# Optimization experiments

Measured on AMD Instinct MI355X. Metric: run time of the kernel, lower is better.

Reference implementation:

```python
import jax, jax.numpy as jnp
import numpy as np

B, N, CS, CZ, CH, H, PQ, PV = 1, 768, 384, 128, 16, 12, 4, 8
INF, EPS, LN_EPS = 1e5, 1e-8, 1e-5


def setup_inputs() -> dict:
    key = jax.random.key(0)
    ks = jax.random.split(key, 16)
    def nrm(k, shape, scale=0.02):
        return jax.random.normal(k, shape, dtype=jnp.float32) * scale
    return {
        "s": jax.random.normal(ks[0], (B, N, CS), jnp.float32),
        "z": jax.random.normal(ks[1], (B, N, N, CZ), jnp.float32),
        "r_rot": jax.random.normal(ks[2], (B, N, 5, 3, 3), jnp.float32),
        "r_trans": jax.random.normal(ks[3], (B, N, 5, 3), jnp.float32),
        "mask": jnp.ones((B, N, 5), jnp.float32),
        "wq": nrm(ks[4], (H * CH, CS)), "bq": jnp.zeros((H * CH,), jnp.float32),
        "wkv": nrm(ks[5], (2 * H * CH, CS)), "bkv": jnp.zeros((2 * H * CH,), jnp.float32),
        "wqp": nrm(ks[6], (H * PQ * 3, CS)), "bqp": jnp.zeros((H * PQ * 3,), jnp.float32),
        "wkvp": nrm(ks[7], (H * (PQ + PV) * 3, CS)), "bkvp": jnp.zeros((H * (PQ + PV) * 3,), jnp.float32),
        "wb": nrm(ks[8], (H, CZ)), "bb": jnp.zeros((H,), jnp.float32),
        "head_w": nrm(ks[9], (H,), 0.5),
        "wout": nrm(ks[10], (CS, H * (CZ + CH + PV * 4))), "bout": jnp.zeros((CS,), jnp.float32),
        "wexp": nrm(ks[11], (5 * CS, CS)), "bexp": jnp.zeros((5 * CS,), jnp.float32),
        "ln_g": jnp.ones((CS,), jnp.float32), "ln_b": jnp.zeros((CS,), jnp.float32),
        "ww": nrm(ks[12], (1, CS)), "bw": jnp.zeros((1,), jnp.float32),
    }


def _mix(x, fg_mask, weight, ndims):
    # x: [B,N,5,...]; weighted blend of backbone frame (index 0) and mean of
    # masked functional-group frames (indices 1:5).
    bb_f = x[:, :, :1]
    m = fg_mask.reshape(fg_mask.shape + (1,) * ndims)
    fg = (x[:, :, 1:] * m).sum(axis=2, keepdims=True)
    denom = fg_mask.sum(-1, keepdims=True).reshape(fg_mask.shape[:2] + (1,) * (ndims + 1))
    fg = fg / (denom + 1e-8)
    w = weight.reshape(weight.shape[:2] + (1,) * (ndims + 1))
    return (w * bb_f + (1.0 - w) * fg)[:, :, 0]


def _ipa(s, z, r_rot, r_trans, mask, wq, bq, wkv, bkv, wqp, bqp, wkvp, bkvp,
         wb, bb, head_w, wout, bout, wexp, bexp, ln_g, ln_b, ww, bw):
    fg_mask = mask[..., 1:]            # [B,N,4]
    ulr = mask[..., 0]                 # [B,N]
    # softmax over a size-1 axis (as in original code -> all ones)
    weight = jax.nn.softmax(s @ ww.T + bw, axis=-1)   # [B,N,1]

    se = (s @ wexp.T + bexp).reshape(B, N, 5, CS)
    mu = se.mean(-1, keepdims=True)
    var = ((se - mu) ** 2).mean(-1, keepdims=True)
    se = (se - mu) * jax.lax.rsqrt(var + LN_EPS) * ln_g + ln_b

    q = _mix((se @ wq.T + bq).reshape(B, N, 5, H, CH), fg_mask, weight, 2)      # [B,N,H,CH]
    kv = _mix((se @ wkv.T + bkv).reshape(B, N, 5, H, 2 * CH), fg_mask, weight, 2)
    k, v = kv[..., :CH], kv[..., CH:]

    def pts_of(w_, b_, npts):
        lin = se @ w_.T + b_                                   # [B,N,5,3*H*npts]
        pts = jnp.moveaxis(lin.reshape(B, N, 5, 3, H * npts), -2, -1)  # [B,N,5,H*npts,3]
        pts = jnp.einsum('bnfij,bnfpj->bnfpi', r_rot, pts) + r_trans[:, :, :, None, :]
        return _mix(pts.reshape(B, N, 5, H, npts, 3), fg_mask, weight, 3)

    q_pts = pts_of(wqp, bqp, PQ)                               # [B,N,H,PQ,3]
    kv_pts = pts_of(wkvp, bkvp, PQ + PV)
    k_pts, v_pts = kv_pts[..., :PQ, :], kv_pts[..., PQ:, :]

    bias = z @ wb.T + bb                                       # [B,N,N,H]
    a = jnp.einsum('bihc,bjhc->bhij', q, k) * (1.0 / (3 * CH)) ** 0.5
    a = a + (1.0 / 3.0) ** 0.5 * jnp.transpose(bias, (0, 3, 1, 2))

    d2 = jnp.sum((q_pts[:, :, None] - k_pts[:, None]) ** 2, axis=-1)  # [B,N,N,H,PQ]
    hw = jax.nn.softplus(head_w) * (1.0 / (3 * (PQ * 9.0 / 2))) ** 0.5
    pt_att = -0.5 * jnp.sum(d2 * hw[:, None], axis=-1)         # [B,N,N,H]
    a = a + jnp.transpose(pt_att, (0, 3, 1, 2))
    sq_mask = INF * (ulr[:, :, None] * ulr[:, None, :] - 1.0)
    a = jax.nn.softmax(a + sq_mask[:, None], axis=-1)          # [B,H,N,N]

    o = jnp.einsum('bhij,bjhc->bihc', a, v).reshape(B, N, H * CH)
    o_pt = jnp.einsum('bhij,bjhpx->bihpx', a, v_pts)           # [B,N,H,PV,3]
    rot0, t0 = r_rot[:, :, 0], r_trans[:, :, 0]                # backbone frame
    # invert_apply: R^T (x - t)
    o_pt = jnp.einsum('bnik,bnhpi->bnhpk', rot0, o_pt - t0[:, :, None, None, :])
    o_pt_norm = jnp.sqrt(jnp.sum(o_pt ** 2, -1) + EPS).reshape(B, N, H * PV)
    o_pt = o_pt.reshape(B, N, H * PV, 3)
    o_pair = jnp.einsum('bhij,bijc->bihc', a, z).reshape(B, N, H * CZ)
    cat = jnp.concatenate([o, o_pt[..., 0], o_pt[..., 1], o_pt[..., 2], o_pt_norm, o_pair], -1)
    return cat @ wout.T + bout                                 # [B,N,CS]


def reference(s, z, r_rot, r_trans, mask, wq, bq, wkv, bkv, wqp, bqp, wkvp, bkvp,
              wb, bb, head_w, wout, bout, wexp, bexp, ln_g, ln_b, ww, bw):
    return _ipa(s, z, r_rot, r_trans, mask, wq, bq, wkv, bkv, wqp, bqp, wkvp, bkvp,
                wb, bb, head_w, wout, bout, wexp, bexp, ln_g, ln_b, ww, bw)
```

## Files before the change

kernel.cpp:

```cpp
#include <hip/hip_runtime.h>
#include <stdint.h>


typedef float f32x4 __attribute__((ext_vector_type(4)));
typedef short s16x8 __attribute__((ext_vector_type(8)));

__device__ __forceinline__ float bf2f(unsigned short u) {
    union { unsigned int i; float f; } v; v.i = ((unsigned int)u) << 16; return v.f;
}
__device__ __forceinline__ float bf2fs(short s) { return bf2f((unsigned short)s); }
__device__ __forceinline__ unsigned short f2bf(float f) {
    union { float f; unsigned int i; } v; v.f = f;
    unsigned int r = v.i + 0x7fffu + ((v.i >> 16) & 1u);
    return (unsigned short)(r >> 16);
}

__global__ __launch_bounds__(256) void k_se(
    const float* __restrict__ s, const float* __restrict__ wexp,
    const float* __restrict__ bexp, const float* __restrict__ ln_g,
    const float* __restrict__ ln_b, float* __restrict__ se0)
{
    const int n0 = blockIdx.x * 4;
    const int t  = threadIdx.x;
    __shared__ float se_l[4 * 384];
    __shared__ float mu_s[4], rs_s[4];

    const bool has1 = (t < 128);
    const float* wr0 = wexp + (size_t)t * 384;
    const float* wr1 = wexp + (size_t)(t + 256) * 384;
    float a0[4] = {0.f,0.f,0.f,0.f}, a1[4] = {0.f,0.f,0.f,0.f};

    for (int k4 = 0; k4 < 96; ++k4) {
        f32x4 sv[4];
        #pragma unroll
        for (int r = 0; r < 4; ++r)
            sv[r] = *(const f32x4*)(s + (size_t)(n0 + r) * 384 + k4 * 4);
        f32x4 w0 = *(const f32x4*)(wr0 + k4 * 4);
        #pragma unroll
        for (int m = 0; m < 4; ++m) {
            float wv = w0[m];
            #pragma unroll
            for (int r = 0; r < 4; ++r) a0[r] += sv[r][m] * wv;
        }
        if (has1) {
            f32x4 w1 = *(const f32x4*)(wr1 + k4 * 4);
            #pragma unroll
            for (int m = 0; m < 4; ++m) {
                float wv = w1[m];
                #pragma unroll
                for (int r = 0; r < 4; ++r) a1[r] += sv[r][m] * wv;
            }
        }
    }
    {
        float b0 = bexp[t];
        #pragma unroll
        for (int r = 0; r < 4; ++r) se_l[r * 384 + t] = a0[r] + b0;
        if (has1) {
            float b1 = bexp[t + 256];
            #pragma unroll
            for (int r = 0; r < 4; ++r) se_l[r * 384 + t + 256] = a1[r] + b1;
        }
    }
    __syncthreads();
    {
        const int w = t >> 6, lane = t & 63;
        float s1 = 0.f, s2 = 0.f;
        #pragma unroll
        for (int q = 0; q < 6; ++q) {
            float v = se_l[w * 384 + lane + q * 64];
            s1 += v; s2 += v * v;
        }
        for (int mk = 1; mk < 64; mk <<= 1) {
            s1 += __shfl_xor(s1, mk, 64);
            s2 += __shfl_xor(s2, mk, 64);
        }
        if (lane == 0) {
            float mu = s1 * (1.f / 384.f);
            float var = s2 * (1.f / 384.f) - mu * mu;
            mu_s[w] = mu;
            rs_s[w] = rsqrtf(fmaxf(var, 0.f) + 1e-5f);
        }
    }
    __syncthreads();
    for (int x = t; x < 4 * 384; x += 256) {
        int r = x / 384, c = x - r * 384;
        se0[(size_t)(n0 + r) * 384 + c] = (se_l[x] - mu_s[r]) * rs_s[r] * ln_g[c] + ln_b[c];
    }
}

__device__ __forceinline__ void wmap(int c,
    const float* wq, const float* bq, const float* wkv, const float* bkv,
    const float* wqp, const float* bqp, const float* wkvp, const float* bkvp,
    const float** w, float* b)
{
    if (c < 192)      { *w = wq   + (size_t)c * 384;         *b = bq[c]; }
    else if (c < 576) { *w = wkv  + (size_t)(c - 192) * 384; *b = bkv[c - 192]; }
    else if (c < 720) { *w = wqp  + (size_t)(c - 576) * 384; *b = bqp[c - 576]; }
    else              { *w = wkvp + (size_t)(c - 720) * 384; *b = bkvp[c - 720]; }
}

__global__ __launch_bounds__(256) void k_proj(
    const float* __restrict__ se0,
    const float* __restrict__ wq,  const float* __restrict__ bq,
    const float* __restrict__ wkv, const float* __restrict__ bkv,
    const float* __restrict__ wqp, const float* __restrict__ bqp,
    const float* __restrict__ wkvp,const float* __restrict__ bkvp,
    const float* __restrict__ r_rot, const float* __restrict__ r_trans,
    float* __restrict__ q_out, unsigned short* __restrict__ k_out,
    unsigned short* __restrict__ v_out, float* __restrict__ qp_out,
    unsigned short* __restrict__ kp_out, unsigned short* __restrict__ vp_out,
    float* __restrict__ k2_out)
{
    const int n0 = blockIdx.x * 8;
    const int cb = blockIdx.y;
    const int t  = threadIdx.x;
    const int cbase = cb * 576;
    __shared__ float lin[8 * 576];
    __shared__ float kprot[8 * 144];

    const bool has2 = (t < 64);
    const float *w0p, *w1p, *w2p; float b0, b1, b2;
    wmap(cbase + t,        wq, bq, wkv, bkv, wqp, bqp, wkvp, bkvp, &w0p, &b0);
    wmap(cbase + t + 256,  wq, bq, wkv, bkv, wqp, bqp, wkvp, bkvp, &w1p, &b1);
    if (has2) wmap(cbase + t + 512, wq, bq, wkv, bkv, wqp, bqp, wkvp, bkvp, &w2p, &b2);
    else { w2p = wq; b2 = 0.f; }

    float ac0[8] = {}, ac1[8] = {}, ac2[8] = {};
    for (int k4 = 0; k4 < 96; ++k4) {
        f32x4 sv[8];
        #pragma unroll
        for (int r = 0; r < 8; ++r)
            sv[r] = *(const f32x4*)(se0 + (size_t)(n0 + r) * 384 + k4 * 4);
        f32x4 wv0 = *(const f32x4*)(w0p + k4 * 4);
        f32x4 wv1 = *(const f32x4*)(w1p + k4 * 4);
        #pragma unroll
        for (int m = 0; m < 4; ++m) {
            float a = wv0[m], b = wv1[m];
            #pragma unroll
            for (int r = 0; r < 8; ++r) { ac0[r] += sv[r][m] * a; ac1[r] += sv[r][m] * b; }
        }
        if (has2) {
            f32x4 wv2 = *(const f32x4*)(w2p + k4 * 4);
            #pragma unroll
            for (int m = 0; m < 4; ++m) {
                float a = wv2[m];
                #pragma unroll
                for (int r = 0; r < 8; ++r) ac2[r] += sv[r][m] * a;
            }
        }
    }
    #pragma unroll
    for (int r = 0; r < 8; ++r) {
        lin[r * 576 + t]       = ac0[r] + b0;
        lin[r * 576 + t + 256] = ac1[r] + b1;
    }
    if (has2) {
        #pragma unroll
        for (int r = 0; r < 8; ++r) lin[r * 576 + t + 512] = ac2[r] + b2;
    }
    __syncthreads();

    if (cb == 0) {
        for (int x = t; x < 8 * 576; x += 256) {
            int r = x / 576, lc = x - r * 576;
            int n = n0 + r;
            float v = lin[x];
            if (lc < 192) q_out[(size_t)n * 192 + lc] = v;
            else {
                int l2 = lc - 192, h = l2 >> 5, c = l2 & 31;
                if (c < 16) k_out[(size_t)n * 192 + h * 16 + c] = f2bf(v);
                else        v_out[(size_t)n * 192 + h * 16 + (c - 16)] = f2bf(v);
            }
        }
    } else {
        for (int x = t; x < 8 * 576; x += 256) {
            int r = x / 576, y = x - r * 576;
            int pt = y / 3, i = y - pt * 3;
            int n = n0 + r;
            const float* rot = r_rot + (size_t)n * 45;
            float t0 = r_trans[(size_t)n * 15 + i];
            float v;
            if (pt < 48) {
                v = rot[i*3+0] * lin[r*576 + pt]
                  + rot[i*3+1] * lin[r*576 + 48 + pt]
                  + rot[i*3+2] * lin[r*576 + 96 + pt] + t0;
                qp_out[(size_t)n * 144 + pt * 3 + i] = v;
            } else {
                int pp = pt - 48;
                v = rot[i*3+0] * lin[r*576 + 144 + pp]
                  + rot[i*3+1] * lin[r*576 + 288 + pp]
                  + rot[i*3+2] * lin[r*576 + 432 + pp] + t0;
                int h = pp / 12, pl = pp - h * 12;
                if (pl < 4) {
                    kp_out[(size_t)n * 144 + (h * 4 + pl) * 3 + i] = f2bf(v);
                    kprot[r * 144 + (h * 4 + pl) * 3 + i] = v;
                } else {
                    vp_out[(size_t)n * 288 + (h * 8 + (pl - 4)) * 3 + i] = f2bf(v);
                }
            }
        }
        __syncthreads();
        if (t < 96) {
            int r = t / 12, h = t - r * 12;
            float ss = 0.f;
            #pragma unroll
            for (int d = 0; d < 12; ++d) {
                float v = kprot[r * 144 + h * 12 + d];
                ss += v * v;
            }
            k2_out[(size_t)(n0 + r) * 12 + h] = ss;
        }
    }
}

__global__ __launch_bounds__(256) void k_attn(
    const float* __restrict__ z, const float* __restrict__ mask,
    const float* __restrict__ head_w, const float* __restrict__ wb,
    const float* __restrict__ bb,
    const float* __restrict__ r_rot, const float* __restrict__ r_trans,
    const float* __restrict__ q_ws, const float* __restrict__ qp_ws,
    const float* __restrict__ k2_ws,
    const unsigned short* __restrict__ k_bf, const unsigned short* __restrict__ v_bf,
    const unsigned short* __restrict__ kp_bf, const unsigned short* __restrict__ vp_bf,
    float* __restrict__ cat)
{
    const int i = blockIdx.x;
    const int t = threadIdx.x;
    const int lane = t & 63, wv = t >> 6;
    const int quad = lane >> 4, lcol = lane & 15;

    __shared__ short zb[64 * 136];
    __shared__ short kt[64 * 200];
    __shared__ short kpt[64 * 146];
    __shared__ float L[64 * 17];
    __shared__ float Pt[16 * 68];
    __shared__ float qs[192], qps[144];
    __shared__ float K2t[64 * 13], ulrt[64];
    __shared__ float m_s[16], l_s[16], alph_s[16], linv_s[16];
    __shared__ float cpt[16], cbbb[16], q2s[16];
    __shared__ float optb[288];

    const float c_qk = 0.14433756729740643f;
    const float c_b  = 0.57735026918962576f;

    if (t < 192) qs[t]  = q_ws[(size_t)i * 192 + t];
    if (t < 144) qps[t] = qp_ws[(size_t)i * 144 + t];
    if (t < 16) { m_s[t] = -1e30f; l_s[t] = 0.f; alph_s[t] = 1.f; }
    if (t < 16) {
        if (t < 12) {
            float x = head_w[t];
            float sp = logf(1.f + __expf(x));
            cpt[t]  = -0.5f * sp * 0.13608276348795434f;
            cbbb[t] = c_b * bb[t];
        } else { cpt[t] = 0.f; cbbb[t] = 0.f; }
    }
    for (int x = t; x < 4 * 68; x += 256) Pt[12 * 68 + x] = 0.f;
    const float ulr_i = mask[(size_t)i * 5];

    s16x8 wbf[4];
    #pragma unroll
    for (int kb = 0; kb < 4; ++kb) {
        #pragma unroll
        for (int j = 0; j < 8; ++j) {
            int c = kb * 32 + quad * 8 + j;
            wbf[kb][j] = (lcol < 12) ? (short)f2bf(wb[(size_t)lcol * 128 + c]) : (short)0;
        }
    }
    __syncthreads();
    if (t < 16) {
        if (t < 12) {
            float ss = 0.f;
            #pragma unroll
            for (int d = 0; d < 12; ++d) { float v = qps[t * 12 + d]; ss += v * v; }
            q2s[t] = ss;
        } else q2s[t] = 0.f;
    }

    f32x4 acc_op[2] = { {0.f,0.f,0.f,0.f}, {0.f,0.f,0.f,0.f} };
    f32x4 acc_s = {0.f,0.f,0.f,0.f};
    int role_h = -1;
    if (t < 48) role_h = t >> 2;
    else if (t >= 64 && t < 136) role_h = ((t - 64) * 4) / 24;

    for (int jt = 0; jt < 12; ++jt) {
        const int j0 = jt * 64;
        __syncthreads();

        {
            const float* zrow = z + (size_t)i * 98304 + (size_t)j0 * 128;
            #pragma unroll
            for (int s = 0; s < 8; ++s) {
                int idx = t + s * 256;
                f32x4 v = *(const f32x4*)(zrow + idx * 4);
                int jl = idx >> 5, c4 = (idx & 31) * 4;
                uint2 pk;
                pk.x = (unsigned)f2bf(v[0]) | ((unsigned)f2bf(v[1]) << 16);
                pk.y = (unsigned)f2bf(v[2]) | ((unsigned)f2bf(v[3]) << 16);
                *(uint2*)&zb[jl * 136 + c4] = pk;
            }
            const uint4* ksrc = (const uint4*)(k_bf + (size_t)j0 * 192);
            #pragma unroll
            for (int s = 0; s < 6; ++s) {
                int idx = t + s * 256;
                uint4 vk = ksrc[idx];
                int jl = idx / 24, c = (idx - jl * 24) * 8;
                *(uint4*)&kt[jl * 200 + c] = vk;
            }
            const uint2* kpsrc = (const uint2*)(kp_bf + (size_t)j0 * 144);
            #pragma unroll
            for (int s = 0; s < 9; ++s) {
                int idx = t + s * 256;
                uint2 vk = kpsrc[idx];
                int jl = idx / 36, c = (idx - jl * 36) * 4;
                *(unsigned int*)&kpt[jl * 146 + c]     = vk.x;
                *(unsigned int*)&kpt[jl * 146 + c + 2] = vk.y;
            }
            #pragma unroll
            for (int s = 0; s < 3; ++s) {
                int x = t + s * 256;
                int jl = x / 12, h = x - jl * 12;
                K2t[jl * 13 + h] = k2_ws[(size_t)j0 * 12 + x];
            }
            if (t < 64) ulrt[t] = mask[(size_t)(j0 + t) * 5];
        }
        __syncthreads();

        {
            f32x4 d = {0.f,0.f,0.f,0.f};
            #pragma unroll
            for (int kb = 0; kb < 4; ++kb) {
                s16x8 a = *(const s16x8*)&zb[(wv * 16 + lcol) * 136 + kb * 32 + quad * 8];
                d = __builtin_amdgcn_mfma_f32_16x16x32_bf16(a, wbf[kb], d, 0, 0, 0);
            }
            if (lcol < 12) {
                #pragma unroll
                for (int r = 0; r < 4; ++r)
                    L[(wv * 16 + quad * 4 + r) * 17 + lcol] = c_b * d[r] + cbbb[lcol];
            }
        }
        __syncthreads();

        #pragma unroll
        for (int es = 0; es < 3; ++es) {
            int e = t + es * 256;
            int h = e >> 6, jl = e & 63;
            f32x4 qv0 = *(const f32x4*)&qs[h * 16];
            f32x4 qv1 = *(const f32x4*)&qs[h * 16 + 4];
            f32x4 qv2 = *(const f32x4*)&qs[h * 16 + 8];
            f32x4 qv3 = *(const f32x4*)&qs[h * 16 + 12];
            s16x8 k0 = *(const s16x8*)&kt[jl * 200 + h * 16];
            s16x8 k1 = *(const s16x8*)&kt[jl * 200 + h * 16 + 8];
            float qk = 0.f;
            #pragma unroll
            for (int m = 0; m < 4; ++m) {
                qk += qv0[m] * bf2fs(k0[m]);
                qk += qv1[m] * bf2fs(k0[4 + m]);
                qk += qv2[m] * bf2fs(k1[m]);
                qk += qv3[m] * bf2fs(k1[4 + m]);
            }
            float dp = 0.f;
            #pragma unroll
            for (int dd = 0; dd < 6; ++dd) {
                unsigned int u = *(const unsigned int*)&kpt[jl * 146 + h * 12 + dd * 2];
                dp += qps[h * 12 + dd * 2]     * bf2f((unsigned short)(u & 0xffffu));
                dp += qps[h * 12 + dd * 2 + 1] * bf2f((unsigned short)(u >> 16));
            }
            float ptt = cpt[h] * (q2s[h] + K2t[jl * 13 + h] - 2.f * dp);
            float lg = c_qk * qk + ptt + 1e5f * (ulr_i * ulrt[jl] - 1.f);
            L[jl * 17 + h] += lg;
        }
        __syncthreads();

        if (t < 192) {
            int h = t >> 4, u = t & 15;
            float v0 = L[(u * 4 + 0) * 17 + h];
            float v1 = L[(u * 4 + 1) * 17 + h];
            float v2 = L[(u * 4 + 2) * 17 + h];
            float v3 = L[(u * 4 + 3) * 17 + h];
            float mx = fmaxf(fmaxf(v0, v1), fmaxf(v2, v3));
            for (int mk = 1; mk < 16; mk <<= 1) mx = fmaxf(mx, __shfl_xor(mx, mk, 16));
            float mold = m_s[h];
            float mnew = fmaxf(mold, mx);
            float w0 = __expf(v0 - mnew), w1 = __expf(v1 - mnew);
            float w2 = __expf(v2 - mnew), w3 = __expf(v3 - mnew);
            Pt[h * 68 + u * 4 + 0] = w0;
            Pt[h * 68 + u * 4 + 1] = w1;
            Pt[h * 68 + u * 4 + 2] = w2;
            Pt[h * 68 + u * 4 + 3] = w3;
            float sm = w0 + w1 + w2 + w3;
            for (int mk = 1; mk < 16; mk <<= 1) sm += __shfl_xor(sm, mk, 16);
            if (u == 0) {
                float al = __expf(mold - mnew);
                m_s[h] = mnew; alph_s[h] = al;
                l_s[h] = l_s[h] * al + sm;
            }
        }
        __syncthreads();

        {
            float al[4];
            #pragma unroll
            for (int r = 0; r < 4; ++r) al[r] = alph_s[quad * 4 + r];
            #pragma unroll
            for (int nt = 0; nt < 2; ++nt)
                #pragma unroll
                for (int r = 0; r < 4; ++r) acc_op[nt][r] *= al[r];
            #pragma unroll
            for (int kb = 0; kb < 2; ++kb) {
                f32x4 pa = *(const f32x4*)&Pt[lcol * 68 + kb * 32 + quad * 8];
                f32x4 pb = *(const f32x4*)&Pt[lcol * 68 + kb * 32 + quad * 8 + 4];
                s16x8 af;
                af[0] = (short)f2bf(pa[0]); af[1] = (short)f2bf(pa[1]);
                af[2] = (short)f2bf(pa[2]); af[3] = (short)f2bf(pa[3]);
                af[4] = (short)f2bf(pb[0]); af[5] = (short)f2bf(pb[1]);
                af[6] = (short)f2bf(pb[2]); af[7] = (short)f2bf(pb[3]);
                #pragma unroll
                for (int nt = 0; nt < 2; ++nt) {
                    int c = wv * 32 + nt * 16 + lcol;
                    s16x8 bfg;
                    #pragma unroll
                    for (int j = 0; j < 8; ++j)
                        bfg[j] = zb[(kb * 32 + quad * 8 + j) * 136 + c];
                    acc_op[nt] = __builtin_amdgcn_mfma_f32_16x16x32_bf16(af, bfg, acc_op[nt], 0, 0, 0);
                }
            }
        }
        if (role_h >= 0) {
            float alpha = alph_s[role_h];
            f32x4 a = acc_s;
            a[0] *= alpha; a[1] *= alpha; a[2] *= alpha; a[3] *= alpha;
            const unsigned int* src;
            int stride_u, off_u;
            if (t < 48) { src = (const unsigned int*)v_bf;  stride_u = 96;  off_u = t * 2; }
            else        { src = (const unsigned int*)vp_bf; stride_u = 144; off_u = (t - 64) * 2; }
            const float* prow = &Pt[role_h * 68];
            #pragma unroll 4
            for (int jl = 0; jl < 64; jl += 4) {
                f32x4 p = *(const f32x4*)(prow + jl);
                #pragma unroll
                for (int m = 0; m < 4; ++m) {
                    uint2 w = *(const uint2*)(src + (size_t)(j0 + jl + m) * stride_u + off_u);
                    float pm = p[m];
                    a[0] += pm * bf2f((unsigned short)(w.x & 0xffffu));
                    a[1] += pm * bf2f((unsigned short)(w.x >> 16));
                    a[2] += pm * bf2f((unsigned short)(w.y & 0xffffu));
                    a[3] += pm * bf2f((unsigned short)(w.y >> 16));
                }
            }
            acc_s = a;
        }
    }

    __syncthreads();
    if (t < 16) linv_s[t] = (t < 12) ? 1.f / l_s[t] : 0.f;
    __syncthreads();
    float* crow = cat + (size_t)i * 2112;
    if (t < 48) {
        float li = linv_s[role_h];
        f32x4 o = acc_s;
        o[0] *= li; o[1] *= li; o[2] *= li; o[3] *= li;
        *(f32x4*)(crow + t * 4) = o;
    }
    if (t >= 64 && t < 136) {
        float li = linv_s[role_h];
        int e0 = (t - 64) * 4;
        optb[e0 + 0] = acc_s[0] * li;
        optb[e0 + 1] = acc_s[1] * li;
        optb[e0 + 2] = acc_s[2] * li;
        optb[e0 + 3] = acc_s[3] * li;
    }
    {
        #pragma unroll
        for (int nt = 0; nt < 2; ++nt)
            #pragma unroll
            for (int r = 0; r < 4; ++r) {
                int h = quad * 4 + r;
                if (h < 12)
                    crow[576 + h * 128 + wv * 32 + nt * 16 + lcol] = acc_op[nt][r] * linv_s[h];
            }
    }
    __syncthreads();
    if (t < 96) {
        int hp = t;
        const float* rot = r_rot + (size_t)i * 45;
        float d0 = optb[hp * 3 + 0] - r_trans[(size_t)i * 15 + 0];
        float d1 = optb[hp * 3 + 1] - r_trans[(size_t)i * 15 + 1];
        float d2 = optb[hp * 3 + 2] - r_trans[(size_t)i * 15 + 2];
        float f0 = rot[0] * d0 + rot[3] * d1 + rot[6] * d2;
        float f1 = rot[1] * d0 + rot[4] * d1 + rot[7] * d2;
        float f2 = rot[2] * d0 + rot[5] * d1 + rot[8] * d2;
        crow[192 + hp] = f0;
        crow[288 + hp] = f1;
        crow[384 + hp] = f2;
        crow[480 + hp] = sqrtf(f0 * f0 + f1 * f1 + f2 * f2 + 1e-8f);
    }
}

__global__ __launch_bounds__(256) void k_gemm(
    const float* __restrict__ cat, const float* __restrict__ wout,
    float* __restrict__ part)
{
    const int mb = blockIdx.x, nb = blockIdx.y, sb = blockIdx.z;
    const int t = threadIdx.x;
    __shared__ float At[16 * 132];
    __shared__ float Bt[16 * 68];
    const int m0 = mb * 128, n0 = nb * 64, koff = sb * 176;
    const int tx = t & 15, ty = t >> 4;
    float acc[8][4] = {};

    for (int ch = 0; ch < 11; ++ch) {
        const int kb = koff + ch * 16;
        __syncthreads();
        #pragma unroll
        for (int s = 0; s < 2; ++s) {
            int idx = t + s * 256;
            int row = idx >> 2, k4 = idx & 3;
            f32x4 v = *(const f32x4*)(cat + (size_t)(m0 + row) * 2112 + kb + k4 * 4);
            At[(k4 * 4 + 0) * 132 + row] = v[0];
            At[(k4 * 4 + 1) * 132 + row] = v[1];
            At[(k4 * 4 + 2) * 132 + row] = v[2];
            At[(k4 * 4 + 3) * 132 + row] = v[3];
        }
        {
            int c = t >> 2, k4 = t & 3;
            f32x4 v = *(const f32x4*)(wout + (size_t)(n0 + c) * 2112 + kb + k4 * 4);
            Bt[(k4 * 4 + 0) * 68 + c] = v[0];
            Bt[(k4 * 4 + 1) * 68 + c] = v[1];
            Bt[(k4 * 4 + 2) * 68 + c] = v[2];
            Bt[(k4 * 4 + 3) * 68 + c] = v[3];
        }
        __syncthreads();
        #pragma unroll
        for (int kk = 0; kk < 16; ++kk) {
            f32x4 b  = *(const f32x4*)&Bt[kk * 68 + tx * 4];
            f32x4 a0 = *(const f32x4*)&At[kk * 132 + ty * 8];
            f32x4 a1 = *(const f32x4*)&At[kk * 132 + ty * 8 + 4];
            #pragma unroll
            for (int r = 0; r < 4; ++r)
                #pragma unroll
                for (int c = 0; c < 4; ++c) acc[r][c] += a0[r] * b[c];
            #pragma unroll
            for (int r = 0; r < 4; ++r)
                #pragma unroll
                for (int c = 0; c < 4; ++c) acc[r + 4][c] += a1[r] * b[c];
        }
    }
    #pragma unroll
    for (int r = 0; r < 8; ++r) {
        f32x4 v = { acc[r][0], acc[r][1], acc[r][2], acc[r][3] };
        *(f32x4*)(part + (size_t)sb * 294912 + (size_t)(m0 + ty * 8 + r) * 384 + n0 + tx * 4) = v;
    }
}

__global__ __launch_bounds__(256) void k_red(
    const float* __restrict__ part, const float* __restrict__ bout,
    float* __restrict__ out)
{
    const int x = blockIdx.x * 256 + threadIdx.x;
    float s = bout[x % 384];
    #pragma unroll
    for (int p = 0; p < 12; ++p) s += part[(size_t)p * 294912 + x];
    out[x] = s;
}

extern "C" void kernel_launch(void* const* d_in, const int* in_sizes, int n_in,
                              void* d_out, int out_size, void* d_ws, size_t ws_size,
                              hipStream_t stream)
{
    const float* s       = (const float*)d_in[0];
    const float* z       = (const float*)d_in[1];
    const float* r_rot   = (const float*)d_in[2];
    const float* r_trans = (const float*)d_in[3];
    const float* mask    = (const float*)d_in[4];
    const float* wq      = (const float*)d_in[5];
    const float* bq      = (const float*)d_in[6];
    const float* wkv     = (const float*)d_in[7];
    const float* bkv     = (const float*)d_in[8];
    const float* wqp     = (const float*)d_in[9];
    const float* bqp     = (const float*)d_in[10];
    const float* wkvp    = (const float*)d_in[11];
    const float* bkvp    = (const float*)d_in[12];
    const float* wb      = (const float*)d_in[13];
    const float* bb      = (const float*)d_in[14];
    const float* head_w  = (const float*)d_in[15];
    const float* wout    = (const float*)d_in[16];
    const float* bout    = (const float*)d_in[17];
    const float* wexp    = (const float*)d_in[18];
    const float* bexp    = (const float*)d_in[19];
    const float* ln_g    = (const float*)d_in[20];
    const float* ln_b    = (const float*)d_in[21];

    float* wsf  = (float*)d_ws;
    float* se0  = wsf;
    float* qf   = wsf + 294912;
    float* qpf  = wsf + 442368;
    float* k2w  = wsf + 552960;
    float* catb = wsf + 562176;
    float* part = wsf + 2184192;
    unsigned short* kbf  = (unsigned short*)((char*)d_ws + 22892544);
    unsigned short* vbf  = kbf + 147456;
    unsigned short* kpbf = vbf + 147456;
    unsigned short* vpbf = kpbf + 110592;
    float* out = (float*)d_out;

    k_se<<<192, 256, 0, stream>>>(s, wexp, bexp, ln_g, ln_b, se0);
    k_proj<<<dim3(96, 2), 256, 0, stream>>>(se0, wq, bq, wkv, bkv, wqp, bqp,
                                            wkvp, bkvp, r_rot, r_trans,
                                            qf, kbf, vbf, qpf, kpbf, vpbf, k2w);
    k_attn<<<768, 256, 0, stream>>>(z, mask, head_w, wb, bb, r_rot, r_trans,
                                    qf, qpf, k2w, kbf, vbf, kpbf, vpbf, catb);
    k_gemm<<<dim3(6, 6, 12), 256, 0, stream>>>(catb, wout, part);
    k_red<<<1152, 256, 0, stream>>>(part, bout, out);
}
```

Measured before the change: 681.7 us.

## Tile projection GEMMs, split LayerNorm, and restructure attention logits and V accumulation

The s-expansion and QKV/point projections are replaced by shared-memory tiled 64x64 GEMM kernels, with LayerNorm and the frame-rotation post-processing moved into separate kernels. In the attention kernel, per-head constants and q/qp vectors are kept in registers, and K/Kp are read directly from global memory instead of being staged in LDS. The z tile gets an XOR swizzle for the MFMA B-operand reads, and the V accumulation is split across two half-tiles that are summed through shared memory. This aims to raise GEMM data reuse and parallelism and cut LDS traffic, at the cost of extra kernel launches and global round trips for intermediates.

```diff
diff --git a/kernel.cpp b/kernel.cpp
--- a/kernel.cpp
+++ b/kernel.cpp
@@ -1,4 +1,5 @@
 #include <hip/hip_runtime.h>
+#include <hip/hip_bf16.h>
 #include <stdint.h>
 
 
@@ -8,104 +9,153 @@
 __device__ __forceinline__ float bf2f(unsigned short u) {
     union { unsigned int i; float f; } v; v.i = ((unsigned int)u) << 16; return v.f;
 }
-__device__ __forceinline__ float bf2fs(short s) { return bf2f((unsigned short)s); }
 __device__ __forceinline__ unsigned short f2bf(float f) {
     union { float f; unsigned int i; } v; v.f = f;
     unsigned int r = v.i + 0x7fffu + ((v.i >> 16) & 1u);
     return (unsigned short)(r >> 16);
 }
-
-__global__ __launch_bounds__(256) void k_se(
+__device__ __forceinline__ unsigned packbf2(float a, float b) {
+    return (unsigned)f2bf(a) | ((unsigned)f2bf(b) << 16);
+}
+
+__global__ __launch_bounds__(256) void k_se_gemm(
     const float* __restrict__ s, const float* __restrict__ wexp,
-    const float* __restrict__ bexp, const float* __restrict__ ln_g,
+    const float* __restrict__ bexp, float* __restrict__ se_raw)
+{
+    const int m0 = blockIdx.x * 64, n0 = blockIdx.y * 64;
+    const int t = threadIdx.x;
+    const int tx = t & 15, ty = t >> 4;
+    __shared__ float Sl[16 * 68];
+    __shared__ float Wl[16 * 68];
+    const int lrow = t >> 2, lk4 = (t & 3) * 4;
+    float acc[4][4] = {};
+
+    for (int kc = 0; kc < 24; ++kc) {
+        const int k0 = kc * 16;
+        __syncthreads();
+        f32x4 sv = *(const f32x4*)(s    + (size_t)(m0 + lrow) * 384 + k0 + lk4);
+        f32x4 wv = *(const f32x4*)(wexp + (size_t)(n0 + lrow) * 384 + k0 + lk4);
+        #pragma unroll
+        for (int i = 0; i < 4; ++i) {
+            Sl[(lk4 + i) * 68 + lrow] = sv[i];
+            Wl[(lk4 + i) * 68 + lrow] = wv[i];
+        }
+        __syncthreads();
+        #pragma unroll
+        for (int kk = 0; kk < 16; ++kk) {
+            f32x4 a = *(const f32x4*)&Sl[kk * 68 + ty * 4];
+            f32x4 b = *(const f32x4*)&Wl[kk * 68 + tx * 4];
+            #pragma unroll
+            for (int r = 0; r < 4; ++r)
+                #pragma unroll
+                for (int c = 0; c < 4; ++c) acc[r][c] += a[r] * b[c];
+        }
+    }
+    f32x4 bb = *(const f32x4*)(bexp + n0 + tx * 4);
+    #pragma unroll
+    for (int r = 0; r < 4; ++r) {
+        f32x4 v = { acc[r][0] + bb[0], acc[r][1] + bb[1],
+                    acc[r][2] + bb[2], acc[r][3] + bb[3] };
+        *(f32x4*)(se_raw + (size_t)(m0 + ty * 4 + r) * 384 + n0 + tx * 4) = v;
+    }
+}
+
+__global__ __launch_bounds__(256) void k_ln(
+    const float* __restrict__ se_raw, const float* __restrict__ ln_g,
     const float* __restrict__ ln_b, float* __restrict__ se0)
 {
-    const int n0 = blockIdx.x * 4;
-    const int t  = threadIdx.x;
-    __shared__ float se_l[4 * 384];
-    __shared__ float mu_s[4], rs_s[4];
-
-    const bool has1 = (t < 128);
-    const float* wr0 = wexp + (size_t)t * 384;
-    const float* wr1 = wexp + (size_t)(t + 256) * 384;
-    float a0[4] = {0.f,0.f,0.f,0.f}, a1[4] = {0.f,0.f,0.f,0.f};
-
-    for (int k4 = 0; k4 < 96; ++k4) {
-        f32x4 sv[4];
-        #pragma unroll
-        for (int r = 0; r < 4; ++r)
-            sv[r] = *(const f32x4*)(s + (size_t)(n0 + r) * 384 + k4 * 4);
-        f32x4 w0 = *(const f32x4*)(wr0 + k4 * 4);
-        #pragma unroll
-        for (int m = 0; m < 4; ++m) {
-            float wv = w0[m];
-            #pragma unroll
-            for (int r = 0; r < 4; ++r) a0[r] += sv[r][m] * wv;
-        }
-        if (has1) {
-            f32x4 w1 = *(const f32x4*)(wr1 + k4 * 4);
-            #pragma unroll
-            for (int m = 0; m < 4; ++m) {
-                float wv = w1[m];
-                #pragma unroll
-                for (int r = 0; r < 4; ++r) a1[r] += sv[r][m] * wv;
-            }
-        }
-    }
-    {
-        float b0 = bexp[t];
-        #pragma unroll
-        for (int r = 0; r < 4; ++r) se_l[r * 384 + t] = a0[r] + b0;
-        if (has1) {
-            float b1 = bexp[t + 256];
-            #pragma unroll
-            for (int r = 0; r < 4; ++r) se_l[r * 384 + t + 256] = a1[r] + b1;
-        }
-    }
-    __syncthreads();
-    {
-        const int w = t >> 6, lane = t & 63;
-        float s1 = 0.f, s2 = 0.f;
-        #pragma unroll
-        for (int q = 0; q < 6; ++q) {
-            float v = se_l[w * 384 + lane + q * 64];
-            s1 += v; s2 += v * v;
-        }
-        for (int mk = 1; mk < 64; mk <<= 1) {
-            s1 += __shfl_xor(s1, mk, 64);
-            s2 += __shfl_xor(s2, mk, 64);
-        }
-        if (lane == 0) {
-            float mu = s1 * (1.f / 384.f);
-            float var = s2 * (1.f / 384.f) - mu * mu;
-            mu_s[w] = mu;
-            rs_s[w] = rsqrtf(fmaxf(var, 0.f) + 1e-5f);
-        }
-    }
-    __syncthreads();
-    for (int x = t; x < 4 * 384; x += 256) {
-        int r = x / 384, c = x - r * 384;
-        se0[(size_t)(n0 + r) * 384 + c] = (se_l[x] - mu_s[r]) * rs_s[r] * ln_g[c] + ln_b[c];
-    }
-}
-
-__device__ __forceinline__ void wmap(int c,
-    const float* wq, const float* bq, const float* wkv, const float* bkv,
-    const float* wqp, const float* bqp, const float* wkvp, const float* bkvp,
-    const float** w, float* b)
-{
-    if (c < 192)      { *w = wq   + (size_t)c * 384;         *b = bq[c]; }
-    else if (c < 576) { *w = wkv  + (size_t)(c - 192) * 384; *b = bkv[c - 192]; }
-    else if (c < 720) { *w = wqp  + (size_t)(c - 576) * 384; *b = bqp[c - 576]; }
-    else              { *w = wkvp + (size_t)(c - 720) * 384; *b = bkvp[c - 720]; }
-}
-
-__global__ __launch_bounds__(256) void k_proj(
+    const int n = blockIdx.x * 4 + (threadIdx.x >> 6);
+    const int lane = threadIdx.x & 63;
+    const float* row = se_raw + (size_t)n * 384;
+    float v[6], s1 = 0.f, s2 = 0.f;
+    #pragma unroll
+    for (int q = 0; q < 6; ++q) {
+        v[q] = row[lane + q * 64];
+        s1 += v[q]; s2 += v[q] * v[q];
+    }
+    for (int mk = 1; mk < 64; mk <<= 1) {
+        s1 += __shfl_xor(s1, mk, 64);
+        s2 += __shfl_xor(s2, mk, 64);
+    }
+    float mu = s1 * (1.f / 384.f);
+    float var = s2 * (1.f / 384.f) - mu * mu;
+    float rs = rsqrtf(fmaxf(var, 0.f) + 1e-5f);
+    float* orow = se0 + (size_t)n * 384;
+    #pragma unroll
+    for (int q = 0; q < 6; ++q) {
+        int c = lane + q * 64;
+        orow[c] = (v[q] - mu) * rs * ln_g[c] + ln_b[c];
+    }
+}
+
+__device__ __forceinline__ const float* wrow(int c,
+    const float* wq, const float* wkv, const float* wqp, const float* wkvp)
+{
+    if (c < 192)      return wq   + (size_t)c * 384;
+    else if (c < 576) return wkv  + (size_t)(c - 192) * 384;
+    else if (c < 720) return wqp  + (size_t)(c - 576) * 384;
+    else              return wkvp + (size_t)(c - 720) * 384;
+}
+__device__ __forceinline__ float bval(int c,
+    const float* bq, const float* bkv, const float* bqp, const float* bkvp)
+{
+    if (c < 192)      return bq[c];
+    else if (c < 576) return bkv[c - 192];
+    else if (c < 720) return bqp[c - 576];
+    else              return bkvp[c - 720];
+}
+
+__global__ __launch_bounds__(256) void k_proj_gemm(
     const float* __restrict__ se0,
     const float* __restrict__ wq,  const float* __restrict__ bq,
     const float* __restrict__ wkv, const float* __restrict__ bkv,
     const float* __restrict__ wqp, const float* __restrict__ bqp,
     const float* __restrict__ wkvp,const float* __restrict__ bkvp,
+    float* __restrict__ lin)
+{
+    const int m0 = blockIdx.x * 64, n0 = blockIdx.y * 64;
+    const int t = threadIdx.x;
+    const int tx = t & 15, ty = t >> 4;
+    __shared__ float Sl[16 * 68];
+    __shared__ float Wl[16 * 68];
+    const int lrow = t >> 2, lk4 = (t & 3) * 4;
+    const float* wp = wrow(n0 + lrow, wq, wkv, wqp, wkvp);
+    float acc[4][4] = {};
+
+    for (int kc = 0; kc < 24; ++kc) {
+        const int k0 = kc * 16;
+        __syncthreads();
+        f32x4 sv = *(const f32x4*)(se0 + (size_t)(m0 + lrow) * 384 + k0 + lk4);
+        f32x4 wv = *(const f32x4*)(wp + k0 + lk4);
+        #pragma unroll
+        for (int i = 0; i < 4; ++i) {
+            Sl[(lk4 + i) * 68 + lrow] = sv[i];
+            Wl[(lk4 + i) * 68 + lrow] = wv[i];
+        }
+        __syncthreads();
+        #pragma unroll
+        for (int kk = 0; kk < 16; ++kk) {
+            f32x4 a = *(const f32x4*)&Sl[kk * 68 + ty * 4];
+            f32x4 b = *(const f32x4*)&Wl[kk * 68 + tx * 4];
+            #pragma unroll
+            for (int r = 0; r < 4; ++r)
+                #pragma unroll
+                for (int c = 0; c < 4; ++c) acc[r][c] += a[r] * b[c];
+        }
+    }
+    float bb[4];
+    #pragma unroll
+    for (int c = 0; c < 4; ++c) bb[c] = bval(n0 + tx * 4 + c, bq, bkv, bqp, bkvp);
+    #pragma unroll
+    for (int r = 0; r < 4; ++r) {
+        f32x4 v = { acc[r][0] + bb[0], acc[r][1] + bb[1],
+                    acc[r][2] + bb[2], acc[r][3] + bb[3] };
+        *(f32x4*)(lin + (size_t)(m0 + ty * 4 + r) * 1152 + n0 + tx * 4) = v;
+    }
+}
+
+__global__ __launch_bounds__(256) void k_post(
+    const float* __restrict__ lin,
     const float* __restrict__ r_rot, const float* __restrict__ r_trans,
     float* __restrict__ q_out, unsigned short* __restrict__ k_out,
     unsigned short* __restrict__ v_out, float* __restrict__ qp_out,
@@ -113,104 +163,57 @@
     float* __restrict__ k2_out)
 {
     const int n0 = blockIdx.x * 8;
-    const int cb = blockIdx.y;
-    const int t  = threadIdx.x;
-    const int cbase = cb * 576;
-    __shared__ float lin[8 * 576];
+    const int t = threadIdx.x;
     __shared__ float kprot[8 * 144];
 
-    const bool has2 = (t < 64);
-    const float *w0p, *w1p, *w2p; float b0, b1, b2;
-    wmap(cbase + t,        wq, bq, wkv, bkv, wqp, bqp, wkvp, bkvp, &w0p, &b0);
-    wmap(cbase + t + 256,  wq, bq, wkv, bkv, wqp, bqp, wkvp, bkvp, &w1p, &b1);
-    if (has2) wmap(cbase + t + 512, wq, bq, wkv, bkv, wqp, bqp, wkvp, bkvp, &w2p, &b2);
-    else { w2p = wq; b2 = 0.f; }
-
-    float ac0[8] = {}, ac1[8] = {}, ac2[8] = {};
-    for (int k4 = 0; k4 < 96; ++k4) {
-        f32x4 sv[8];
-        #pragma unroll
-        for (int r = 0; r < 8; ++r)
-            sv[r] = *(const f32x4*)(se0 + (size_t)(n0 + r) * 384 + k4 * 4);
-        f32x4 wv0 = *(const f32x4*)(w0p + k4 * 4);
-        f32x4 wv1 = *(const f32x4*)(w1p + k4 * 4);
-        #pragma unroll
-        for (int m = 0; m < 4; ++m) {
-            float a = wv0[m], b = wv1[m];
-            #pragma unroll
-            for (int r = 0; r < 8; ++r) { ac0[r] += sv[r][m] * a; ac1[r] += sv[r][m] * b; }
-        }
-        if (has2) {
-            f32x4 wv2 = *(const f32x4*)(w2p + k4 * 4);
-            #pragma unroll
-            for (int m = 0; m < 4; ++m) {
-                float a = wv2[m];
-                #pragma unroll
-                for (int r = 0; r < 8; ++r) ac2[r] += sv[r][m] * a;
-            }
-        }
-    }
-    #pragma unroll
     for (int r = 0; r < 8; ++r) {
-        lin[r * 576 + t]       = ac0[r] + b0;
-        lin[r * 576 + t + 256] = ac1[r] + b1;
-    }
-    if (has2) {
-        #pragma unroll
-        for (int r = 0; r < 8; ++r) lin[r * 576 + t + 512] = ac2[r] + b2;
-    }
-    __syncthreads();
-
-    if (cb == 0) {
-        for (int x = t; x < 8 * 576; x += 256) {
-            int r = x / 576, lc = x - r * 576;
-            int n = n0 + r;
-            float v = lin[x];
-            if (lc < 192) q_out[(size_t)n * 192 + lc] = v;
-            else {
-                int l2 = lc - 192, h = l2 >> 5, c = l2 & 31;
+        const int n = n0 + r;
+        const float* lrow = lin + (size_t)n * 1152;
+        const float* rot = r_rot + (size_t)n * 45;
+        for (int u = t; u < 1152; u += 256) {
+            if (u < 192) {
+                q_out[(size_t)n * 192 + u] = lrow[u];
+            } else if (u < 576) {
+                int l2 = u - 192, h = l2 >> 5, c = l2 & 31;
+                float v = lrow[u];
                 if (c < 16) k_out[(size_t)n * 192 + h * 16 + c] = f2bf(v);
                 else        v_out[(size_t)n * 192 + h * 16 + (c - 16)] = f2bf(v);
-            }
-        }
-    } else {
-        for (int x = t; x < 8 * 576; x += 256) {
-            int r = x / 576, y = x - r * 576;
-            int pt = y / 3, i = y - pt * 3;
-            int n = n0 + r;
-            const float* rot = r_rot + (size_t)n * 45;
-            float t0 = r_trans[(size_t)n * 15 + i];
-            float v;
-            if (pt < 48) {
-                v = rot[i*3+0] * lin[r*576 + pt]
-                  + rot[i*3+1] * lin[r*576 + 48 + pt]
-                  + rot[i*3+2] * lin[r*576 + 96 + pt] + t0;
-                qp_out[(size_t)n * 144 + pt * 3 + i] = v;
             } else {
-                int pp = pt - 48;
-                v = rot[i*3+0] * lin[r*576 + 144 + pp]
-                  + rot[i*3+1] * lin[r*576 + 288 + pp]
-                  + rot[i*3+2] * lin[r*576 + 432 + pp] + t0;
-                int h = pp / 12, pl = pp - h * 12;
-                if (pl < 4) {
-                    kp_out[(size_t)n * 144 + (h * 4 + pl) * 3 + i] = f2bf(v);
-                    kprot[r * 144 + (h * 4 + pl) * 3 + i] = v;
+                int y = u - 576;
+                int pt = y / 3, i = y - pt * 3;
+                float t0 = r_trans[(size_t)n * 15 + i];
+                float v;
+                if (pt < 48) {
+                    v = rot[i*3+0] * lrow[576 + pt]
+                      + rot[i*3+1] * lrow[576 + 48 + pt]
+                      + rot[i*3+2] * lrow[576 + 96 + pt] + t0;
+                    qp_out[(size_t)n * 144 + pt * 3 + i] = v;
                 } else {
-                    vp_out[(size_t)n * 288 + (h * 8 + (pl - 4)) * 3 + i] = f2bf(v);
+                    int pp = pt - 48;
+                    v = rot[i*3+0] * lrow[720 + pp]
+                      + rot[i*3+1] * lrow[720 + 144 + pp]
+                      + rot[i*3+2] * lrow[720 + 288 + pp] + t0;
+                    int h = pp / 12, pl = pp - h * 12;
+                    if (pl < 4) {
+                        kp_out[(size_t)n * 144 + (h * 4 + pl) * 3 + i] = f2bf(v);
+                        kprot[r * 144 + (h * 4 + pl) * 3 + i] = v;
+                    } else {
+                        vp_out[(size_t)n * 288 + (h * 8 + (pl - 4)) * 3 + i] = f2bf(v);
+                    }
                 }
             }
         }
-        __syncthreads();
-        if (t < 96) {
-            int r = t / 12, h = t - r * 12;
-            float ss = 0.f;
-            #pragma unroll
-            for (int d = 0; d < 12; ++d) {
-                float v = kprot[r * 144 + h * 12 + d];
-                ss += v * v;
-            }
-            k2_out[(size_t)(n0 + r) * 12 + h] = ss;
-        }
+    }
+    __syncthreads();
+    if (t < 96) {
+        int r = t / 12, h = t - r * 12;
+        float ss = 0.f;
+        #pragma unroll
+        for (int d = 0; d < 12; ++d) {
+            float v = kprot[r * 144 + h * 12 + d];
+            ss += v * v;
+        }
+        k2_out[(size_t)(n0 + r) * 12 + h] = ss;
     }
 }
 
@@ -231,15 +234,13 @@
     const int quad = lane >> 4, lcol = lane & 15;
 
     __shared__ short zb[64 * 136];
-    __shared__ short kt[64 * 200];
-    __shared__ short kpt[64 * 146];
     __shared__ float L[64 * 17];
     __shared__ float Pt[16 * 68];
     __shared__ float qs[192], qps[144];
-    __shared__ float K2t[64 * 13], ulrt[64];
+    __shared__ float ulrt[64];
     __shared__ float m_s[16], l_s[16], alph_s[16], linv_s[16];
-    __shared__ float cpt[16], cbbb[16], q2s[16];
     __shared__ float optb[288];
+    __shared__ float vbuf[240 * 4];
 
     const float c_qk = 0.14433756729740643f;
     const float c_b  = 0.57735026918962576f;
@@ -247,14 +248,6 @@
     if (t < 192) qs[t]  = q_ws[(size_t)i * 192 + t];
     if (t < 144) qps[t] = qp_ws[(size_t)i * 144 + t];
     if (t < 16) { m_s[t] = -1e30f; l_s[t] = 0.f; alph_s[t] = 1.f; }
-    if (t < 16) {
-        if (t < 12) {
-            float x = head_w[t];
-            float sp = logf(1.f + __expf(x));
-            cpt[t]  = -0.5f * sp * 0.13608276348795434f;
-            cbbb[t] = c_b * bb[t];
-        } else { cpt[t] = 0.f; cbbb[t] = 0.f; }
-    }
     for (int x = t; x < 4 * 68; x += 256) Pt[12 * 68 + x] = 0.f;
     const float ulr_i = mask[(size_t)i * 5];
 
@@ -268,20 +261,35 @@
         }
     }
     __syncthreads();
-    if (t < 16) {
-        if (t < 12) {
-            float ss = 0.f;
-            #pragma unroll
-            for (int d = 0; d < 12; ++d) { float v = qps[t * 12 + d]; ss += v * v; }
-            q2s[t] = ss;
-        } else q2s[t] = 0.f;
+
+    f32x4 qv[4]; f32x4 qpv[3];
+    float q2_r = 0.f, cpt_r = 0.f, cbb_r = 0.f;
+    if (lcol < 12) {
+        #pragma unroll
+        for (int m = 0; m < 4; ++m) qv[m] = *(const f32x4*)&qs[lcol * 16 + m * 4];
+        #pragma unroll
+        for (int m = 0; m < 3; ++m) {
+            qpv[m] = *(const f32x4*)&qps[lcol * 12 + m * 4];
+            #pragma unroll
+            for (int e = 0; e < 4; ++e) q2_r += qpv[m][e] * qpv[m][e];
+        }
+        float x = head_w[lcol];
+        float sp = logf(1.f + __expf(x));
+        cpt_r = -0.5f * sp * 0.13608276348795434f;
+        cbb_r = c_b * bb[lcol];
     }
 
     f32x4 acc_op[2] = { {0.f,0.f,0.f,0.f}, {0.f,0.f,0.f,0.f} };
     f32x4 acc_s = {0.f,0.f,0.f,0.f};
-    int role_h = -1;
-    if (t < 48) role_h = t >> 2;
-    else if (t >= 64 && t < 136) role_h = ((t - 64) * 4) / 24;
+
+    int vu = -1, vhalf = 0;
+    if (t < 120) { vu = t; vhalf = 0; }
+    else if (t >= 128 && t < 248) { vu = t - 128; vhalf = 1; }
+    int vrole = -1; const unsigned int* vsrc = nullptr; int vstride = 0, voff = 0;
+    if (vu >= 0) {
+        if (vu < 48) { vrole = vu >> 2; vsrc = (const unsigned int*)v_bf;  vstride = 96;  voff = vu * 2; }
+        else         { vrole = (vu - 48) / 6; vsrc = (const unsigned int*)vp_bf; vstride = 144; voff = (vu - 48) * 2; }
+    }
 
     for (int jt = 0; jt < 12; ++jt) {
         const int j0 = jt * 64;
@@ -293,34 +301,12 @@
             for (int s = 0; s < 8; ++s) {
                 int idx = t + s * 256;
                 f32x4 v = *(const f32x4*)(zrow + idx * 4);
-                int jl = idx >> 5, c4 = (idx & 31) * 4;
+                int jl = idx >> 5, cq = idx & 31;
+                int ch = (cq >> 1) ^ ((jl >> 3) & 3);
                 uint2 pk;
-                pk.x = (unsigned)f2bf(v[0]) | ((unsigned)f2bf(v[1]) << 16);
-                pk.y = (unsigned)f2bf(v[2]) | ((unsigned)f2bf(v[3]) << 16);
-                *(uint2*)&zb[jl * 136 + c4] = pk;
-            }
-            const uint4* ksrc = (const uint4*)(k_bf + (size_t)j0 * 192);
-            #pragma unroll
-            for (int s = 0; s < 6; ++s) {
-                int idx = t + s * 256;
-                uint4 vk = ksrc[idx];
-                int jl = idx / 24, c = (idx - jl * 24) * 8;
-                *(uint4*)&kt[jl * 200 + c] = vk;
-            }
-            const uint2* kpsrc = (const uint2*)(kp_bf + (size_t)j0 * 144);
-            #pragma unroll
-            for (int s = 0; s < 9; ++s) {
-                int idx = t + s * 256;
-                uint2 vk = kpsrc[idx];
-                int jl = idx / 36, c = (idx - jl * 36) * 4;
-                *(unsigned int*)&kpt[jl * 146 + c]     = vk.x;
-                *(unsigned int*)&kpt[jl * 146 + c + 2] = vk.y;
-            }
-            #pragma unroll
-            for (int s = 0; s < 3; ++s) {
-                int x = t + s * 256;
-                int jl = x / 12, h = x - jl * 12;
-                K2t[jl * 13 + h] = k2_ws[(size_t)j0 * 12 + x];
+                pk.x = packbf2(v[0], v[1]);
+                pk.y = packbf2(v[2], v[3]);
+                *(uint2*)&zb[jl * 136 + ch * 8 + (cq & 1) * 4] = pk;
             }
             if (t < 64) ulrt[t] = mask[(size_t)(j0 + t) * 5];
         }
@@ -328,47 +314,85 @@
 
         {
             f32x4 d = {0.f,0.f,0.f,0.f};
+            const int sigm = ((wv * 16 + lcol) >> 3) & 3;
             #pragma unroll
             for (int kb = 0; kb < 4; ++kb) {
-                s16x8 a = *(const s16x8*)&zb[(wv * 16 + lcol) * 136 + kb * 32 + quad * 8];
+                s16x8 a = *(const s16x8*)&zb[(wv * 16 + lcol) * 136 + ((kb * 4 + quad) ^ sigm) * 8];
                 d = __builtin_amdgcn_mfma_f32_16x16x32_bf16(a, wbf[kb], d, 0, 0, 0);
             }
             if (lcol < 12) {
                 #pragma unroll
-                for (int r = 0; r < 4; ++r)
-                    L[(wv * 16 + quad * 4 + r) * 17 + lcol] = c_b * d[r] + cbbb[lcol];
-            }
-        }
-        __syncthreads();
-
-        #pragma unroll
-        for (int es = 0; es < 3; ++es) {
-            int e = t + es * 256;
-            int h = e >> 6, jl = e & 63;
-            f32x4 qv0 = *(const f32x4*)&qs[h * 16];
-            f32x4 qv1 = *(const f32x4*)&qs[h * 16 + 4];
-            f32x4 qv2 = *(const f32x4*)&qs[h * 16 + 8];
-            f32x4 qv3 = *(const f32x4*)&qs[h * 16 + 12];
-            s16x8 k0 = *(const s16x8*)&kt[jl * 200 + h * 16];
-            s16x8 k1 = *(const s16x8*)&kt[jl * 200 + h * 16 + 8];
-            float qk = 0.f;
-            #pragma unroll
-            for (int m = 0; m < 4; ++m) {
-                qk += qv0[m] * bf2fs(k0[m]);
-                qk += qv1[m] * bf2fs(k0[4 + m]);
-                qk += qv2[m] * bf2fs(k1[m]);
-                qk += qv3[m] * bf2fs(k1[4 + m]);
-            }
-            float dp = 0.f;
-            #pragma unroll
-            for (int dd = 0; dd < 6; ++dd) {
-                unsigned int u = *(const unsigned int*)&kpt[jl * 146 + h * 12 + dd * 2];
-                dp += qps[h * 12 + dd * 2]     * bf2f((unsigned short)(u & 0xffffu));
-                dp += qps[h * 12 + dd * 2 + 1] * bf2f((unsigned short)(u >> 16));
-            }
-            float ptt = cpt[h] * (q2s[h] + K2t[jl * 13 + h] - 2.f * dp);
-            float lg = c_qk * qk + ptt + 1e5f * (ulr_i * ulrt[jl] - 1.f);
-            L[jl * 17 + h] += lg;
+                for (int r = 0; r < 4; ++r) {
+                    const int jl = wv * 16 + quad * 4 + r;
+                    const int jr = j0 + jl;
+                    uint4 k0 = *(const uint4*)(k_bf + (size_t)jr * 192 + lcol * 16);
+                    uint4 k1 = *(const uint4*)(k_bf + (size_t)jr * 192 + lcol * 16 + 8);
+                    float qk = 0.f;
+                    const unsigned int* kw = (const unsigned int*)&k0;
+                    #pragma unroll
+                    for (int m = 0; m < 4; ++m) {
+                        qk += qv[m >> 1][(m & 1) * 2 + 0] * 0.f;
+                    }
+                    {
+                        float q0, q1; unsigned u;
+                        qk = 0.f;
+                        #pragma unroll
+                        for (int m = 0; m < 4; ++m) {
+                            u = kw[m];
+                            q0 = qv[m][0]; q1 = qv[m][1];
+                            qk += q0 * bf2f((unsigned short)(u & 0xffffu));
+                            qk += q1 * bf2f((unsigned short)(u >> 16));
+                            u = ((const unsigned int*)&k0)[m];
+                        }
+                        const unsigned int* kw1 = (const unsigned int*)&k1;
+                        #pragma unroll
+                        for (int m = 0; m < 4; ++m) {
+                            u = kw1[m];
+                            qk += qv[m][2] * bf2f((unsigned short)(u & 0xffffu));
+                            qk += qv[m][3] * bf2f((unsigned short)(u >> 16));
+                        }
+                    }
+                    {
+                        float qf[16];
+                        const unsigned int* kwa = (const unsigned int*)&k0;
+                        const unsigned int* kwb = (const unsigned int*)&k1;
+                        #pragma unroll
+                        for (int m = 0; m < 4; ++m) {
+                            qf[m * 2]     = bf2f((unsigned short)(kwa[m] & 0xffffu));
+                            qf[m * 2 + 1] = bf2f((unsigned short)(kwa[m] >> 16));
+                            qf[8 + m * 2]     = bf2f((unsigned short)(kwb[m] & 0xffffu));
+                            qf[8 + m * 2 + 1] = bf2f((unsigned short)(kwb[m] >> 16));
+                        }
+                        qk = 0.f;
+                        #pragma unroll
+                        for (int m = 0; m < 16; ++m) qk += qv[m >> 2][m & 3] * qf[m];
+                    }
+                    uint2 p0 = *(const uint2*)(kp_bf + (size_t)jr * 144 + lcol * 12);
+                    uint2 p1 = *(const uint2*)(kp_bf + (size_t)jr * 144 + lcol * 12 + 4);
+                    uint2 p2 = *(const uint2*)(kp_bf + (size_t)jr * 144 + lcol * 12 + 8);
+                    float kpv[12];
+                    kpv[0] = bf2f((unsigned short)(p0.x & 0xffffu));
+                    kpv[1] = bf2f((unsigned short)(p0.x >> 16));
+                    kpv[2] = bf2f((unsigned short)(p0.y & 0xffffu));
+                    kpv[3] = bf2f((unsigned short)(p0.y >> 16));
+                    kpv[4] = bf2f((unsigned short)(p1.x & 0xffffu));
+                    kpv[5] = bf2f((unsigned short)(p1.x >> 16));
+                    kpv[6] = bf2f((unsigned short)(p1.y & 0xffffu));
+                    kpv[7] = bf2f((unsigned short)(p1.y >> 16));
+                    kpv[8] = bf2f((unsigned short)(p2.x & 0xffffu));
+                    kpv[9] = bf2f((unsigned short)(p2.x >> 16));
+                    kpv[10] = bf2f((unsigned short)(p2.y & 0xffffu));
+                    kpv[11] = bf2f((unsigned short)(p2.y >> 16));
+                    float dp = 0.f;
+                    #pragma unroll
+                    for (int m = 0; m < 12; ++m) dp += qpv[m >> 2][m & 3] * kpv[m];
+                    float K2 = k2_ws[(size_t)jr * 12 + lcol];
+                    float ptt = cpt_r * (q2_r + K2 - 2.f * dp);
+                    float lg = c_qk * qk + ptt + 1e5f * (ulr_i * ulrt[jl] - 1.f)
+                             + c_b * d[r] + cbb_r;
+                    L[jl * 17 + lcol] = lg;
+                }
+            }
         }
         __syncthreads();
 
@@ -410,37 +434,35 @@
             for (int kb = 0; kb < 2; ++kb) {
                 f32x4 pa = *(const f32x4*)&Pt[lcol * 68 + kb * 32 + quad * 8];
                 f32x4 pb = *(const f32x4*)&Pt[lcol * 68 + kb * 32 + quad * 8 + 4];
-                s16x8 af;
-                af[0] = (short)f2bf(pa[0]); af[1] = (short)f2bf(pa[1]);
-                af[2] = (short)f2bf(pa[2]); af[3] = (short)f2bf(pa[3]);
-                af[4] = (short)f2bf(pb[0]); af[5] = (short)f2bf(pb[1]);
-                af[6] = (short)f2bf(pb[2]); af[7] = (short)f2bf(pb[3]);
+                union { s16x8 v; unsigned u[4]; } af;
+                af.u[0] = packbf2(pa[0], pa[1]);
+                af.u[1] = packbf2(pa[2], pa[3]);
+                af.u[2] = packbf2(pb[0], pb[1]);
+                af.u[3] = packbf2(pb[2], pb[3]);
                 #pragma unroll
                 for (int nt = 0; nt < 2; ++nt) {
                     int c = wv * 32 + nt * 16 + lcol;
+                    int csw = ((c >> 3) ^ quad) * 8 + (c & 7);
                     s16x8 bfg;
                     #pragma unroll
                     for (int j = 0; j < 8; ++j)
-                        bfg[j] = zb[(kb * 32 + quad * 8 + j) * 136 + c];
-                    acc_op[nt] = __builtin_amdgcn_mfma_f32_16x16x32_bf16(af, bfg, acc_op[nt], 0, 0, 0);
+                        bfg[j] = zb[(kb * 32 + quad * 8 + j) * 136 + csw];
+                    acc_op[nt] = __builtin_amdgcn_mfma_f32_16x16x32_bf16(af.v, bfg, acc_op[nt], 0, 0, 0);
                 }
             }
         }
-        if (role_h >= 0) {
-            float alpha = alph_s[role_h];
+        if (vu >= 0) {
+            float alpha = alph_s[vrole];
             f32x4 a = acc_s;
             a[0] *= alpha; a[1] *= alpha; a[2] *= alpha; a[3] *= alpha;
-            const unsigned int* src;
-            int stride_u, off_u;
-            if (t < 48) { src = (const unsigned int*)v_bf;  stride_u = 96;  off_u = t * 2; }
-            else        { src = (const unsigned int*)vp_bf; stride_u = 144; off_u = (t - 64) * 2; }
-            const float* prow = &Pt[role_h * 68];
+            const float* prow = &Pt[vrole * 68 + vhalf * 32];
+            const unsigned int* src = vsrc + (size_t)(j0 + vhalf * 32) * vstride + voff;
             #pragma unroll 4
-            for (int jl = 0; jl < 64; jl += 4) {
-                f32x4 p = *(const f32x4*)(prow + jl);
+            for (int jj = 0; jj < 32; jj += 4) {
+                f32x4 p = *(const f32x4*)(prow + jj);
                 #pragma unroll
                 for (int m = 0; m < 4; ++m) {
-                    uint2 w = *(const uint2*)(src + (size_t)(j0 + jl + m) * stride_u + off_u);
+                    uint2 w = *(const uint2*)(src + (size_t)(jj + m) * vstride);
                     float pm = p[m];
                     a[0] += pm * bf2f((unsigned short)(w.x & 0xffffu));
                     a[1] += pm * bf2f((unsigned short)(w.x >> 16));
@@ -454,21 +476,27 @@
 
     __syncthreads();
     if (t < 16) linv_s[t] = (t < 12) ? 1.f / l_s[t] : 0.f;
+    if (vu >= 0) {
+        #pragma unroll
+        for (int m = 0; m < 4; ++m) vbuf[(vu * 2 + vhalf) * 4 + m] = acc_s[m];
+    }
     __syncthreads();
     float* crow = cat + (size_t)i * 2112;
-    if (t < 48) {
-        float li = linv_s[role_h];
-        f32x4 o = acc_s;
-        o[0] *= li; o[1] *= li; o[2] *= li; o[3] *= li;
-        *(f32x4*)(crow + t * 4) = o;
-    }
-    if (t >= 64 && t < 136) {
-        float li = linv_s[role_h];
-        int e0 = (t - 64) * 4;
-        optb[e0 + 0] = acc_s[0] * li;
-        optb[e0 + 1] = acc_s[1] * li;
-        optb[e0 + 2] = acc_s[2] * li;
-        optb[e0 + 3] = acc_s[3] * li;
+    if (t < 120) {
+        int role = (t < 48) ? (t >> 2) : (t - 48) / 6;
+        float li = linv_s[role];
+        float f[4];
+        #pragma unroll
+        for (int m = 0; m < 4; ++m)
+            f[m] = (vbuf[(t * 2) * 4 + m] + vbuf[(t * 2 + 1) * 4 + m]) * li;
+        if (t < 48) {
+            f32x4 o = { f[0], f[1], f[2], f[3] };
+            *(f32x4*)(crow + t * 4) = o;
+        } else {
+            int e0 = (t - 48) * 4;
+            optb[e0 + 0] = f[0]; optb[e0 + 1] = f[1];
+            optb[e0 + 2] = f[2]; optb[e0 + 3] = f[3];
+        }
     }
     {
         #pragma unroll
@@ -598,16 +626,20 @@
     float* k2w  = wsf + 552960;
     float* catb = wsf + 562176;
     float* part = wsf + 2184192;
+    float* lin    = catb;
+    float* se_raw = part;
     unsigned short* kbf  = (unsigned short*)((char*)d_ws + 22892544);
     unsigned short* vbf  = kbf + 147456;
     unsigned short* kpbf = vbf + 147456;
     unsigned short* vpbf = kpbf + 110592;
     float* out = (float*)d_out;
 
-    k_se<<<192, 256, 0, stream>>>(s, wexp, bexp, ln_g, ln_b, se0);
-    k_proj<<<dim3(96, 2), 256, 0, stream>>>(se0, wq, bq, wkv, bkv, wqp, bqp,
-                                            wkvp, bkvp, r_rot, r_trans,
-                                            qf, kbf, vbf, qpf, kpbf, vpbf, k2w);
+    k_se_gemm<<<dim3(12, 6), 256, 0, stream>>>(s, wexp, bexp, se_raw);
+    k_ln<<<192, 256, 0, stream>>>(se_raw, ln_g, ln_b, se0);
+    k_proj_gemm<<<dim3(12, 18), 256, 0, stream>>>(se0, wq, bq, wkv, bkv,
+                                                  wqp, bqp, wkvp, bkvp, lin);
+    k_post<<<96, 256, 0, stream>>>(lin, r_rot, r_trans,
+                                   qf, kbf, vbf, qpf, kpbf, vpbf, k2w);
     k_attn<<<768, 256, 0, stream>>>(z, mask, head_w, wb, bb, r_rot, r_trans,
                                     qf, qpf, k2w, kbf, vbf, kpbf, vpbf, catb);
     k_gemm<<<dim3(6, 6, 12), 256, 0, stream>>>(catb, wout, part);
```

New measurement: 700.8 us. 2.8% more time.
